# Kernel optimization log

Measured on AMD Instinct MI355X. Metric: run time of the kernel, lower is better.

Reference implementation:

```python
import jax, jax.numpy as jnp
import numpy as np

N_ACT = 300000
C = 128
K = 9
BATCH, H, W = 4, 1024, 1024
EPS = 1e-4  # scn BatchNormalization default eps


def _build_rulebook(rng):
    # sample N_ACT unique active sites on a (BATCH, H, W) grid
    flat = np.sort(rng.choice(BATCH * H * W, size=N_ACT, replace=False).astype(np.int64))
    b = flat // (H * W)
    y = (flat // W) % H
    x = flat % W
    nbr = np.full((N_ACT, K), -1, dtype=np.int32)
    k = 0
    for dy in (-1, 0, 1):
        for dx in (-1, 0, 1):
            ny, nx = y + dy, x + dx
            valid = (ny >= 0) & (ny < H) & (nx >= 0) & (nx < W)
            nflat = b * (H * W) + ny * W + nx
            pos = np.searchsorted(flat, nflat)
            pos_c = np.clip(pos, 0, N_ACT - 1)
            found = valid & (flat[pos_c] == nflat)
            nbr[:, k] = np.where(found, pos_c, -1).astype(np.int32)
            k += 1
    return jnp.asarray(nbr)


def setup_inputs() -> dict:
    key = jax.random.key(0)
    k1, k2, k3 = jax.random.split(key, 3)
    rng = np.random.default_rng(0)
    nbr_idx = _build_rulebook(rng)
    scale = 1.0 / np.sqrt(K * C)
    return {
        "x": jax.random.normal(k1, (N_ACT, C), dtype=jnp.float32),
        "nbr_idx": nbr_idx,
        "W1": jax.random.normal(k2, (K, C, C), dtype=jnp.float32) * scale,
        "gamma1": jnp.ones((C,), jnp.float32),
        "beta1": jnp.zeros((C,), jnp.float32),
        "W2": jax.random.normal(k3, (K, C, C), dtype=jnp.float32) * scale,
        "gamma2": jnp.ones((C,), jnp.float32),
        "beta2": jnp.zeros((C,), jnp.float32),
    }


def _subm_conv(feats, nbr_idx, Wk):
    # gather -> GEMM -> accumulate, one pass per kernel offset (K=9 fixed)
    out = jnp.zeros((feats.shape[0], Wk.shape[2]), feats.dtype)
    for k in range(Wk.shape[0]):
        idx = nbr_idx[:, k]
        mask = (idx >= 0)[:, None]
        g = jnp.where(mask, feats[jnp.maximum(idx, 0)], 0.0)
        out = out + g @ Wk[k]
    return out


def _batchnorm(feats, gamma, beta):
    mean = feats.mean(axis=0)
    var = feats.var(axis=0)  # biased, as in torch BN normalization
    return (feats - mean) * jax.lax.rsqrt(var + EPS) * gamma + beta


def reference(x, nbr_idx, W1, gamma1, beta1, W2, gamma2, beta2):
    out = _subm_conv(x, nbr_idx, W1)
    out = jax.nn.relu(_batchnorm(out, gamma1, beta1))  # BatchNormReLU
    out = _subm_conv(out, nbr_idx, W2)
    out = _batchnorm(out, gamma2, beta2)  # BatchNormalization
    return jax.nn.relu(out + x)  # AddTable + ReLU
```

## Files before the change

### kernel.cpp

```cpp
#include <hip/hip_runtime.h>


#define N_ACT 300000
#define NTAP  9
#define EPSV  1e-4f

using f16x8 = __attribute__((ext_vector_type(8))) _Float16;
using f32x4 = __attribute__((ext_vector_type(4))) float;

#define OFF_PH    0UL
#define OFF_TMP   76800000UL
#define OFF_W1    230400000UL
#define OFF_W2    (OFF_W1 + 294912UL)
#define OFF_STATS (OFF_W2 + 294912UL)
#define OFF_ZBUF  (OFF_STATS + 2048UL)
#define OFF_SB    (OFF_ZBUF + 256UL)

__device__ __forceinline__ unsigned short f2h(float v) {
  _Float16 h = (_Float16)v;
  return __builtin_bit_cast(unsigned short, h);
}

__global__ void prep_kernel(const float* __restrict__ W1, const float* __restrict__ W2,
                            unsigned short* __restrict__ w1, unsigned short* __restrict__ w2,
                            float* __restrict__ zstats) {
  int b = blockIdx.x, t = threadIdx.x;
  if (b == 36) {
    for (int i = t; i < 576; i += 256) zstats[i] = 0.f;
    return;
  }
  int w = b / 18, rem = b % 18;
  int tap = rem >> 1, ch = rem & 1;
  const float* W = w ? W2 : W1;
  unsigned short* o = w ? w2 : w1;
  int n  = t >> 1;
  int s0 = (t & 1) * 4;
  for (int s = s0; s < s0 + 4; ++s) {
    int sigma = s ^ (n & 7);
    for (int j = 0; j < 8; ++j) {
      int   k = ch * 64 + sigma * 8 + j;
      float v = W[tap * 16384 + k * 128 + n];
      o[rem * 8192 + n * 64 + s * 8 + j] = f2h(v);
    }
  }
}

__global__ void tohalf_kernel(const float* __restrict__ x, unsigned short* __restrict__ ph) {
  int i = (blockIdx.x * 256 + threadIdx.x) * 8;
  float4 a = *(const float4*)(x + i);
  float4 b = *(const float4*)(x + i + 4);
  uint4 p;
  p.x = (unsigned)f2h(a.x) | ((unsigned)f2h(a.y) << 16);
  p.y = (unsigned)f2h(a.z) | ((unsigned)f2h(a.w) << 16);
  p.z = (unsigned)f2h(b.x) | ((unsigned)f2h(b.y) << 16);
  p.w = (unsigned)f2h(b.z) | ((unsigned)f2h(b.w) << 16);
  *(uint4*)(ph + i) = p;
}

__global__ __launch_bounds__(256, 4)
void conv_kernel(const unsigned short* __restrict__ pH, const int* __restrict__ nbr,
                 const unsigned short* __restrict__ wH,
                 float* __restrict__ outp, float* __restrict__ ssum, float* __restrict__ ssq,
                 const unsigned short* __restrict__ zbuf) {
  __shared__ char smem[32768];
  const int t  = threadIdx.x;
  const int wv = t >> 6, ln = t & 63;
  const int m0 = blockIdx.x * 128;
  const int rs = ln >> 3, sg = ln & 7;
  const int lane16 = ln & 15, g = ln >> 4;

  f32x4 acc[16];
#pragma unroll
  for (int i = 0; i < 16; ++i) acc[i] = f32x4{0.f, 0.f, 0.f, 0.f};

  for (int tap = 0; tap < NTAP; ++tap) {
    int idx4[4];
#pragma unroll
    for (int it = 0; it < 4; ++it) {
      int gm = m0 + wv * 32 + it * 8 + rs;
      idx4[it] = (gm < N_ACT) ? nbr[gm * 9 + tap] : -1;
    }
#pragma unroll
    for (int ch = 0; ch < 2; ++ch) {
      __syncthreads();
#pragma unroll
      for (int it = 0; it < 4; ++it) {
        int r     = wv * 32 + it * 8 + rs;
        int sigma = sg ^ (r & 7);
        int idx   = idx4[it];
        long off  = (long)(idx >= 0 ? idx : 0) * 128 + ch * 64 + sigma * 8;
        const unsigned short* gs = (idx >= 0) ? (pH + off) : (zbuf + sigma * 8);
        int lo = r * 128 + sg * 16;
        __builtin_amdgcn_global_load_lds((const __attribute__((address_space(1))) void*)gs,
                                         (__attribute__((address_space(3))) void*)(smem + lo), 16, 0, 0);
      }
      {
        const char* gb = (const char*)wH + (tap * 2 + ch) * 16384;
#pragma unroll
        for (int it = 0; it < 4; ++it) {
          int o = wv * 4096 + it * 1024 + ln * 16;
          __builtin_amdgcn_global_load_lds((const __attribute__((address_space(1))) void*)(gb + o),
                                           (__attribute__((address_space(3))) void*)(smem + 16384 + o), 16, 0, 0);
        }
      }
      __syncthreads();
#pragma unroll
      for (int ks = 0; ks < 2; ++ks) {
        f16x8 ah[4], bh[4];
        int sigma = ks * 4 + g;
#pragma unroll
        for (int mt = 0; mt < 4; ++mt) {
          int m = (wv & 1) * 64 + mt * 16 + lane16;
          ah[mt] = *(const f16x8*)(smem + m * 128 + ((sigma ^ (m & 7)) * 16));
        }
#pragma unroll
        for (int nt = 0; nt < 4; ++nt) {
          int n = (wv >> 1) * 64 + nt * 16 + lane16;
          bh[nt] = *(const f16x8*)(smem + 16384 + n * 128 + ((sigma ^ (n & 7)) * 16));
        }
#pragma unroll
        for (int mt = 0; mt < 4; ++mt)
#pragma unroll
          for (int nt = 0; nt < 4; ++nt)
            acc[mt * 4 + nt] = __builtin_amdgcn_mfma_f32_16x16x32_f16(ah[mt], bh[nt], acc[mt * 4 + nt], 0, 0, 0);
      }
    }
  }
  int rowbase = m0 + (wv & 1) * 64;
  int colbase = (wv >> 1) * 64;
  float s[4], q[4];
#pragma unroll
  for (int nt = 0; nt < 4; ++nt) { s[nt] = 0.f; q[nt] = 0.f; }
#pragma unroll
  for (int mt = 0; mt < 4; ++mt)
#pragma unroll
    for (int nt = 0; nt < 4; ++nt)
#pragma unroll
      for (int r = 0; r < 4; ++r) {
        float v  = acc[mt * 4 + nt][r];
        int  row = rowbase + mt * 16 + g * 4 + r;
        int  col = colbase + nt * 16 + lane16;
        if (row < N_ACT) outp[row * 128 + col] = v;
        s[nt] += v; q[nt] += v * v;
      }
  __syncthreads();
  float* sbuf = (float*)smem;
  float* qbuf = ((float*)smem) + 256;
#pragma unroll
  for (int nt = 0; nt < 4; ++nt) {
    float sv = s[nt], qv = q[nt];
    sv += __shfl_xor(sv, 16, 64); sv += __shfl_xor(sv, 32, 64);
    qv += __shfl_xor(qv, 16, 64); qv += __shfl_xor(qv, 32, 64);
    if (ln < 16) { sbuf[wv * 64 + nt * 16 + ln] = sv; qbuf[wv * 64 + nt * 16 + ln] = qv; }
  }
  __syncthreads();
  if (t < 128) {
    int c = t;
    float tot = (c < 64) ? (sbuf[c] + sbuf[64 + c]) : (sbuf[128 + (c - 64)] + sbuf[192 + (c - 64)]);
    atomicAdd(ssum + c, tot);
  } else {
    int c = t - 128;
    float tot = (c < 64) ? (qbuf[c] + qbuf[64 + c]) : (qbuf[128 + (c - 64)] + qbuf[192 + (c - 64)]);
    atomicAdd(ssq + c, tot);
  }
}

__global__ void finalize_stats_kernel(const float* __restrict__ ssum, const float* __restrict__ ssq,
                                      const float* __restrict__ gamma, const float* __restrict__ beta,
                                      float* __restrict__ scale, float* __restrict__ bias) {
  int c = threadIdx.x;
  float mean = ssum[c] * (1.f / N_ACT);
  float var  = ssq[c] * (1.f / N_ACT) - mean * mean;
  float sc   = rsqrtf(var + EPSV) * gamma[c];
  scale[c] = sc;
  bias[c]  = beta[c] - mean * sc;
}

__global__ void bn_relu_tohalf_kernel(const float* __restrict__ tmp,
                                      const float* __restrict__ scale, const float* __restrict__ bias,
                                      unsigned short* __restrict__ ph) {
  int i = (blockIdx.x * 256 + threadIdx.x) * 8;
  int c = i & 127;
  float4 v0 = *(const float4*)(tmp + i);
  float4 v1 = *(const float4*)(tmp + i + 4);
  float4 s0 = *(const float4*)(scale + c);
  float4 s1 = *(const float4*)(scale + c + 4);
  float4 b0 = *(const float4*)(bias + c);
  float4 b1 = *(const float4*)(bias + c + 4);
  float y0 = fmaxf(v0.x * s0.x + b0.x, 0.f);
  float y1 = fmaxf(v0.y * s0.y + b0.y, 0.f);
  float y2 = fmaxf(v0.z * s0.z + b0.z, 0.f);
  float y3 = fmaxf(v0.w * s0.w + b0.w, 0.f);
  float y4 = fmaxf(v1.x * s1.x + b1.x, 0.f);
  float y5 = fmaxf(v1.y * s1.y + b1.y, 0.f);
  float y6 = fmaxf(v1.z * s1.z + b1.z, 0.f);
  float y7 = fmaxf(v1.w * s1.w + b1.w, 0.f);
  uint4 p;
  p.x = (unsigned)f2h(y0) | ((unsigned)f2h(y1) << 16);
  p.y = (unsigned)f2h(y2) | ((unsigned)f2h(y3) << 16);
  p.z = (unsigned)f2h(y4) | ((unsigned)f2h(y5) << 16);
  p.w = (unsigned)f2h(y6) | ((unsigned)f2h(y7) << 16);
  *(uint4*)(ph + i) = p;
}

__global__ void final_kernel(const float* __restrict__ tmp,
                             const float* __restrict__ scale, const float* __restrict__ bias,
                             const float* __restrict__ x, float* __restrict__ outp) {
  int i = (blockIdx.x * 256 + threadIdx.x) * 4;
  int c = i & 127;
  float4 v  = *(const float4*)(tmp + i);
  float4 sc = *(const float4*)(scale + c);
  float4 bs = *(const float4*)(bias + c);
  float4 xx = *(const float4*)(x + i);
  float4 o;
  o.x = fmaxf(v.x * sc.x + bs.x + xx.x, 0.f);
  o.y = fmaxf(v.y * sc.y + bs.y + xx.y, 0.f);
  o.z = fmaxf(v.z * sc.z + bs.z + xx.z, 0.f);
  o.w = fmaxf(v.w * sc.w + bs.w + xx.w, 0.f);
  *(float4*)(outp + i) = o;
}

extern "C" void kernel_launch(void* const* d_in, const int* in_sizes, int n_in,
                              void* d_out, int out_size, void* d_ws, size_t ws_size,
                              hipStream_t stream) {
  const float* x   = (const float*)d_in[0];
  const int*   nbr = (const int*)d_in[1];
  const float* W1  = (const float*)d_in[2];
  const float* g1  = (const float*)d_in[3];
  const float* b1  = (const float*)d_in[4];
  const float* W2  = (const float*)d_in[5];
  const float* g2  = (const float*)d_in[6];
  const float* b2  = (const float*)d_in[7];
  float* out = (float*)d_out;
  char*  ws  = (char*)d_ws;

  unsigned short* ph  = (unsigned short*)(ws + OFF_PH);
  float*          tmp = (float*)(ws + OFF_TMP);
  unsigned short* w1  = (unsigned short*)(ws + OFF_W1);
  unsigned short* w2  = (unsigned short*)(ws + OFF_W2);
  float*          st  = (float*)(ws + OFF_STATS);
  unsigned short* zb  = (unsigned short*)(ws + OFF_ZBUF);
  float*          sc  = (float*)(ws + OFF_SB);
  float*          bi  = sc + 128;

  prep_kernel<<<37, 256, 0, stream>>>(W1, W2, w1, w2, st);
  tohalf_kernel<<<18750, 256, 0, stream>>>(x, ph);
  conv_kernel<<<2344, 256, 0, stream>>>(ph, nbr, w1, tmp, st, st + 128, zb);
  finalize_stats_kernel<<<1, 128, 0, stream>>>(st, st + 128, g1, b1, sc, bi);
  bn_relu_tohalf_kernel<<<18750, 256, 0, stream>>>(tmp, sc, bi, ph);
  conv_kernel<<<2344, 256, 0, stream>>>(ph, nbr, w2, tmp, st + 256, st + 384, zb);
  finalize_stats_kernel<<<1, 128, 0, stream>>>(st + 256, st + 384, g2, b2, sc, bi);
  final_kernel<<<37500, 256, 0, stream>>>(tmp, sc, bi, x, out);
}
```

Before: 590.1 us.

## Double-buffer conv gather/weight loads and store conv output as fp16

The conv kernel now preloads all nine neighbour indices and double-buffers the gathered activations and weights in 64KB of LDS. The global-to-LDS copy for the next chunk is issued before the MFMA compute on the current one, so load latency can overlap compute. The intermediate conv output is stored as fp16 instead of fp32, halving its write and read traffic in the BN and final kernels, and the final kernel now handles 8 elements per thread. Occupancy drops (launch bounds 4→2, more LDS), and the fp16 intermediate adds rounding error before the batchnorm.

After: 569.9 us. 3.4% less time.

```diff
diff --git a/kernel.cpp b/kernel.cpp
--- a/kernel.cpp
+++ b/kernel.cpp
@@ -57,75 +57,93 @@
   *(uint4*)(ph + i) = p;
 }
 
-__global__ __launch_bounds__(256, 4)
+__global__ __launch_bounds__(256, 2)
 void conv_kernel(const unsigned short* __restrict__ pH, const int* __restrict__ nbr,
                  const unsigned short* __restrict__ wH,
-                 float* __restrict__ outp, float* __restrict__ ssum, float* __restrict__ ssq,
+                 unsigned short* __restrict__ outp, float* __restrict__ ssum, float* __restrict__ ssq,
                  const unsigned short* __restrict__ zbuf) {
-  __shared__ char smem[32768];
+  __shared__ char smem[65536];
   const int t  = threadIdx.x;
   const int wv = t >> 6, ln = t & 63;
   const int m0 = blockIdx.x * 128;
   const int rs = ln >> 3, sg = ln & 7;
   const int lane16 = ln & 15, g = ln >> 4;
 
-  f32x4 acc[16];
-#pragma unroll
-  for (int i = 0; i < 16; ++i) acc[i] = f32x4{0.f, 0.f, 0.f, 0.f};
-
-  for (int tap = 0; tap < NTAP; ++tap) {
-    int idx4[4];
+  int idx[NTAP][4];
+#pragma unroll
+  for (int tap = 0; tap < NTAP; ++tap)
 #pragma unroll
     for (int it = 0; it < 4; ++it) {
       int gm = m0 + wv * 32 + it * 8 + rs;
-      idx4[it] = (gm < N_ACT) ? nbr[gm * 9 + tap] : -1;
-    }
-#pragma unroll
-    for (int ch = 0; ch < 2; ++ch) {
-      __syncthreads();
-#pragma unroll
-      for (int it = 0; it < 4; ++it) {
-        int r     = wv * 32 + it * 8 + rs;
-        int sigma = sg ^ (r & 7);
-        int idx   = idx4[it];
-        long off  = (long)(idx >= 0 ? idx : 0) * 128 + ch * 64 + sigma * 8;
-        const unsigned short* gs = (idx >= 0) ? (pH + off) : (zbuf + sigma * 8);
-        int lo = r * 128 + sg * 16;
-        __builtin_amdgcn_global_load_lds((const __attribute__((address_space(1))) void*)gs,
-                                         (__attribute__((address_space(3))) void*)(smem + lo), 16, 0, 0);
+      idx[tap][it] = (gm < N_ACT) ? nbr[gm * 9 + tap] : -1;
+    }
+
+  f32x4 acc[16];
+#pragma unroll
+  for (int i = 0; i < 16; ++i) acc[i] = f32x4{0.f, 0.f, 0.f, 0.f};
+
+  auto stage = [&](int c, int p) {
+    const int tap = c >> 1, ch = c & 1;
+#pragma unroll
+    for (int it = 0; it < 4; ++it) {
+      int r     = wv * 32 + it * 8 + rs;
+      int sigma = sg ^ (r & 7);
+      int id    = idx[tap][it];
+      long off  = (long)(id >= 0 ? id : 0) * 128 + ch * 64 + sigma * 8;
+      const unsigned short* gs = (id >= 0) ? (pH + off) : (zbuf + sigma * 8);
+      int lo = p * 16384 + r * 128 + sg * 16;
+      __builtin_amdgcn_global_load_lds((const __attribute__((address_space(1))) void*)gs,
+                                       (__attribute__((address_space(3))) void*)(smem + lo), 16, 0, 0);
+    }
+    const char* gb = (const char*)wH + (tap * 2 + ch) * 16384;
+#pragma unroll
+    for (int it = 0; it < 4; ++it) {
+      int o = wv * 4096 + it * 1024 + ln * 16;
+      __builtin_amdgcn_global_load_lds((const __attribute__((address_space(1))) void*)(gb + o),
+                                       (__attribute__((address_space(3))) void*)(smem + 32768 + p * 16384 + o), 16, 0, 0);
+    }
+  };
+
+  auto compute = [&](int p) {
+    const char* bufA = smem + p * 16384;
+    const char* bufB = smem + 32768 + p * 16384;
+#pragma unroll
+    for (int ks = 0; ks < 2; ++ks) {
+      f16x8 ah[4], bh[4];
+      int sigma = ks * 4 + g;
+#pragma unroll
+      for (int mt = 0; mt < 4; ++mt) {
+        int m = (wv & 1) * 64 + mt * 16 + lane16;
+        ah[mt] = *(const f16x8*)(bufA + m * 128 + ((sigma ^ (m & 7)) * 16));
       }
-      {
-        const char* gb = (const char*)wH + (tap * 2 + ch) * 16384;
-#pragma unroll
-        for (int it = 0; it < 4; ++it) {
-          int o = wv * 4096 + it * 1024 + ln * 16;
-          __builtin_amdgcn_global_load_lds((const __attribute__((address_space(1))) void*)(gb + o),
-                                           (__attribute__((address_space(3))) void*)(smem + 16384 + o), 16, 0, 0);
-        }
+#pragma unroll
+      for (int nt = 0; nt < 4; ++nt) {
+        int n = (wv >> 1) * 64 + nt * 16 + lane16;
+        bh[nt] = *(const f16x8*)(bufB + n * 128 + ((sigma ^ (n & 7)) * 16));
       }
-      __syncthreads();
-#pragma unroll
-      for (int ks = 0; ks < 2; ++ks) {
-        f16x8 ah[4], bh[4];
-        int sigma = ks * 4 + g;
-#pragma unroll
-        for (int mt = 0; mt < 4; ++mt) {
-          int m = (wv & 1) * 64 + mt * 16 + lane16;
-          ah[mt] = *(const f16x8*)(smem + m * 128 + ((sigma ^ (m & 7)) * 16));
-        }
-#pragma unroll
-        for (int nt = 0; nt < 4; ++nt) {
-          int n = (wv >> 1) * 64 + nt * 16 + lane16;
-          bh[nt] = *(const f16x8*)(smem + 16384 + n * 128 + ((sigma ^ (n & 7)) * 16));
-        }
-#pragma unroll
-        for (int mt = 0; mt < 4; ++mt)
-#pragma unroll
-          for (int nt = 0; nt < 4; ++nt)
-            acc[mt * 4 + nt] = __builtin_amdgcn_mfma_f32_16x16x32_f16(ah[mt], bh[nt], acc[mt * 4 + nt], 0, 0, 0);
-      }
-    }
-  }
+#pragma unroll
+      for (int mt = 0; mt < 4; ++mt)
+#pragma unroll
+        for (int nt = 0; nt < 4; ++nt)
+          acc[mt * 4 + nt] = __builtin_amdgcn_mfma_f32_16x16x32_f16(ah[mt], bh[nt], acc[mt * 4 + nt], 0, 0, 0);
+    }
+  };
+
+  stage(0, 0);
+  asm volatile("s_waitcnt vmcnt(0)" ::: "memory");
+  __builtin_amdgcn_sched_barrier(0);
+  __builtin_amdgcn_s_barrier();
+
+#pragma unroll
+  for (int c = 0; c < 17; ++c) {
+    stage(c + 1, (c + 1) & 1);
+    compute(c & 1);
+    asm volatile("s_waitcnt vmcnt(0)" ::: "memory");
+    __builtin_amdgcn_sched_barrier(0);
+    __builtin_amdgcn_s_barrier();
+  }
+  compute(1);
+
   int rowbase = m0 + (wv & 1) * 64;
   int colbase = (wv >> 1) * 64;
   float s[4], q[4];
@@ -140,7 +158,7 @@
         float v  = acc[mt * 4 + nt][r];
         int  row = rowbase + mt * 16 + g * 4 + r;
         int  col = colbase + nt * 16 + lane16;
-        if (row < N_ACT) outp[row * 128 + col] = v;
+        if (row < N_ACT) outp[row * 128 + col] = f2h(v);
         s[nt] += v; q[nt] += v * v;
       }
   __syncthreads();
@@ -176,25 +194,24 @@
   bias[c]  = beta[c] - mean * sc;
 }
 
-__global__ void bn_relu_tohalf_kernel(const float* __restrict__ tmp,
+__global__ void bn_relu_tohalf_kernel(const unsigned short* __restrict__ tmp,
                                       const float* __restrict__ scale, const float* __restrict__ bias,
                                       unsigned short* __restrict__ ph) {
   int i = (blockIdx.x * 256 + threadIdx.x) * 8;
   int c = i & 127;
-  float4 v0 = *(const float4*)(tmp + i);
-  float4 v1 = *(const float4*)(tmp + i + 4);
+  f16x8 v = *(const f16x8*)(tmp + i);
   float4 s0 = *(const float4*)(scale + c);
   float4 s1 = *(const float4*)(scale + c + 4);
   float4 b0 = *(const float4*)(bias + c);
   float4 b1 = *(const float4*)(bias + c + 4);
-  float y0 = fmaxf(v0.x * s0.x + b0.x, 0.f);
-  float y1 = fmaxf(v0.y * s0.y + b0.y, 0.f);
-  float y2 = fmaxf(v0.z * s0.z + b0.z, 0.f);
-  float y3 = fmaxf(v0.w * s0.w + b0.w, 0.f);
-  float y4 = fmaxf(v1.x * s1.x + b1.x, 0.f);
-  float y5 = fmaxf(v1.y * s1.y + b1.y, 0.f);
-  float y6 = fmaxf(v1.z * s1.z + b1.z, 0.f);
-  float y7 = fmaxf(v1.w * s1.w + b1.w, 0.f);
+  float y0 = fmaxf((float)v[0] * s0.x + b0.x, 0.f);
+  float y1 = fmaxf((float)v[1] * s0.y + b0.y, 0.f);
+  float y2 = fmaxf((float)v[2] * s0.z + b0.z, 0.f);
+  float y3 = fmaxf((float)v[3] * s0.w + b0.w, 0.f);
+  float y4 = fmaxf((float)v[4] * s1.x + b1.x, 0.f);
+  float y5 = fmaxf((float)v[5] * s1.y + b1.y, 0.f);
+  float y6 = fmaxf((float)v[6] * s1.z + b1.z, 0.f);
+  float y7 = fmaxf((float)v[7] * s1.w + b1.w, 0.f);
   uint4 p;
   p.x = (unsigned)f2h(y0) | ((unsigned)f2h(y1) << 16);
   p.y = (unsigned)f2h(y2) | ((unsigned)f2h(y3) << 16);
@@ -203,21 +220,29 @@
   *(uint4*)(ph + i) = p;
 }
 
-__global__ void final_kernel(const float* __restrict__ tmp,
+__global__ void final_kernel(const unsigned short* __restrict__ tmp,
                              const float* __restrict__ scale, const float* __restrict__ bias,
                              const float* __restrict__ x, float* __restrict__ outp) {
-  int i = (blockIdx.x * 256 + threadIdx.x) * 4;
+  int i = (blockIdx.x * 256 + threadIdx.x) * 8;
   int c = i & 127;
-  float4 v  = *(const float4*)(tmp + i);
-  float4 sc = *(const float4*)(scale + c);
-  float4 bs = *(const float4*)(bias + c);
-  float4 xx = *(const float4*)(x + i);
-  float4 o;
-  o.x = fmaxf(v.x * sc.x + bs.x + xx.x, 0.f);
-  o.y = fmaxf(v.y * sc.y + bs.y + xx.y, 0.f);
-  o.z = fmaxf(v.z * sc.z + bs.z + xx.z, 0.f);
-  o.w = fmaxf(v.w * sc.w + bs.w + xx.w, 0.f);
-  *(float4*)(outp + i) = o;
+  f16x8 v = *(const f16x8*)(tmp + i);
+  float4 s0 = *(const float4*)(scale + c);
+  float4 s1 = *(const float4*)(scale + c + 4);
+  float4 b0 = *(const float4*)(bias + c);
+  float4 b1 = *(const float4*)(bias + c + 4);
+  float4 x0 = *(const float4*)(x + i);
+  float4 x1 = *(const float4*)(x + i + 4);
+  float4 o0, o1;
+  o0.x = fmaxf((float)v[0] * s0.x + b0.x + x0.x, 0.f);
+  o0.y = fmaxf((float)v[1] * s0.y + b0.y + x0.y, 0.f);
+  o0.z = fmaxf((float)v[2] * s0.z + b0.z + x0.z, 0.f);
+  o0.w = fmaxf((float)v[3] * s0.w + b0.w + x0.w, 0.f);
+  o1.x = fmaxf((float)v[4] * s1.x + b1.x + x1.x, 0.f);
+  o1.y = fmaxf((float)v[5] * s1.y + b1.y + x1.y, 0.f);
+  o1.z = fmaxf((float)v[6] * s1.z + b1.z + x1.z, 0.f);
+  o1.w = fmaxf((float)v[7] * s1.w + b1.w + x1.w, 0.f);
+  *(float4*)(outp + i) = o0;
+  *(float4*)(outp + i + 4) = o1;
 }
 
 extern "C" void kernel_launch(void* const* d_in, const int* in_sizes, int n_in,
@@ -235,7 +260,7 @@
   char*  ws  = (char*)d_ws;
 
   unsigned short* ph  = (unsigned short*)(ws + OFF_PH);
-  float*          tmp = (float*)(ws + OFF_TMP);
+  unsigned short* tmp = (unsigned short*)(ws + OFF_TMP);
   unsigned short* w1  = (unsigned short*)(ws + OFF_W1);
   unsigned short* w2  = (unsigned short*)(ws + OFF_W2);
   float*          st  = (float*)(ws + OFF_STATS);
@@ -250,5 +275,5 @@
   bn_relu_tohalf_kernel<<<18750, 256, 0, stream>>>(tmp, sc, bi, ph);
   conv_kernel<<<2344, 256, 0, stream>>>(ph, nbr, w2, tmp, st + 256, st + 384, zb);
   finalize_stats_kernel<<<1, 128, 0, stream>>>(st + 256, st + 384, g2, b2, sc, bi);
-  final_kernel<<<37500, 256, 0, stream>>>(tmp, sc, bi, x, out);
-}
+  final_kernel<<<18750, 256, 0, stream>>>(tmp, sc, bi, x, out);
+}
```
